# Performance work log

Hardware: AMD Instinct MI355X
Metric: run time of the kernel (lower is better)

The kernel has to match this reference:

```python
import jax, jax.numpy as jnp
import numpy as np


def setup_inputs() -> dict:
    key = jax.random.key(0)
    k1, k2 = jax.random.split(key)
    B, F, D = 4096, 32, 64
    P = F * (F - 1) // 2  # 496
    inputs = jax.random.normal(k1, (B, F, D), dtype=jnp.float32)
    W = jax.random.normal(k2, (P, D, D), dtype=jnp.float32) * 0.05
    return {"inputs": inputs, "W": W}


def reference(inputs, W):
    # inputs: (B, F, D); W: (P, D, D) with P = F*(F-1)/2 pairs in
    # itertools.combinations order (== np.triu_indices row-major order).
    F = inputs.shape[1]
    idx_i, idx_j = np.triu_indices(F, k=1)  # static pair indices
    vi = inputs[:, idx_i, :]                 # (B, P, D)
    vj = inputs[:, idx_j, :]                 # (B, P, D)
    # per-pair matmul v_i @ W_p, then elementwise multiply with v_j
    vidots = jnp.einsum('bpd,pde->bpe', vi, W)
    return vidots * vj                       # (B, P, D)
```

## Files before the change

kernel.cpp:

```cpp
#include <hip/hip_runtime.h>

#define Bsz 4096
#define Fsz 32
#define Dsz 64
#define Psz 496
#define RPW 64
#define WPB 4

__global__ __launch_bounds__(256, 4)
void bilinear_wreg_kernel(const float* __restrict__ in,
                          const float* __restrict__ W,
                          float* __restrict__ out)
{
    const int p    = blockIdx.x;
    const int tid  = threadIdx.x;
    const int lane = tid & 63;

    const int bb0 = __builtin_amdgcn_readfirstlane(
                        blockIdx.y * (RPW * WPB) + (tid >> 6) * RPW);

    int i = 0, rem = p;
    while (rem >= Fsz - 1 - i) { rem -= Fsz - 1 - i; ++i; }
    const int j = i + 1 + rem;

    float w[Dsz];
    {
        const float* Wp = W + (size_t)p * (Dsz * Dsz) + lane;
#pragma unroll
        for (int d = 0; d < Dsz; ++d) w[d] = Wp[(size_t)d * Dsz];
    }
#pragma unroll
    for (int d = 0; d < Dsz; ++d) {
        asm volatile("" : "+v"(w[d]));
    }

    const float* __restrict__ vi0 = in  + ((size_t)bb0 * Fsz + i) * Dsz;
    const float* __restrict__ vj0 = in  + ((size_t)bb0 * Fsz + j) * Dsz + lane;
    float*       __restrict__ op0 = out + ((size_t)bb0 * Psz + p) * Dsz + lane;

#pragma unroll 1
    for (int r = 0; r < RPW; ++r) {
        const float* vi  = vi0 + (size_t)r * (Fsz * Dsz);
        const float  vjv = vj0[(size_t)r * (Fsz * Dsz)];

        float s[Dsz];
#pragma unroll
        for (int d = 0; d < Dsz; ++d) s[d] = vi[d];

        float acc = 0.0f;
#pragma unroll
        for (int d = 0; d < Dsz; ++d) acc = fmaf(s[d], w[d], acc);

        __builtin_nontemporal_store(acc * vjv, op0 + (size_t)r * (Psz * Dsz));
    }
}

extern "C" void kernel_launch(void* const* d_in, const int* in_sizes, int n_in,
                              void* d_out, int out_size, void* d_ws, size_t ws_size,
                              hipStream_t stream) {
    const float* in  = (const float*)d_in[0];
    const float* W   = (const float*)d_in[1];
    float*       out = (float*)d_out;

    dim3 grid(Psz, Bsz / (RPW * WPB));
    bilinear_wreg_kernel<<<grid, 256, 0, stream>>>(in, W, out);
}
```

Before: 747.1 us.

## Stage W in shared memory and block over rows to cut register use

Stops holding the 64 W entries per lane in registers. Each block now copies the pair's W matrix into LDS with float4 loads and then reads it in chunks of eight. The loop processes eight batch rows at a time with separate accumulators, so each W chunk is reused across those rows. Launch bounds go from 4 to 8 blocks per CU to raise occupancy. In exchange the kernel adds LDS reads, a barrier, and 16KB of LDS per block, which may limit how many blocks fit on a CU.

New measurement: 1.320 ms. 76.6% more time.

```diff
diff --git a/kernel.cpp b/kernel.cpp
--- a/kernel.cpp
+++ b/kernel.cpp
@@ -6,12 +6,16 @@
 #define Psz 496
 #define RPW 64
 #define WPB 4
+#define RB  8
+#define DC  8
 
-__global__ __launch_bounds__(256, 4)
-void bilinear_wreg_kernel(const float* __restrict__ in,
+__global__ __launch_bounds__(256, 8)
+void bilinear_sblk_kernel(const float* __restrict__ in,
                           const float* __restrict__ W,
                           float* __restrict__ out)
 {
+    __shared__ float sW[Dsz][Dsz];
+
     const int p    = blockIdx.x;
     const int tid  = threadIdx.x;
     const int lane = tid & 63;
@@ -23,35 +27,45 @@
     while (rem >= Fsz - 1 - i) { rem -= Fsz - 1 - i; ++i; }
     const int j = i + 1 + rem;
 
-    float w[Dsz];
     {
-        const float* Wp = W + (size_t)p * (Dsz * Dsz) + lane;
+        const float4* gW  = (const float4*)(W + (size_t)p * Dsz * Dsz);
+        float4*       sWv = (float4*)(&sW[0][0]);
 #pragma unroll
-        for (int d = 0; d < Dsz; ++d) w[d] = Wp[(size_t)d * Dsz];
+        for (int k = 0; k < 4; ++k) sWv[tid + k * 256] = gW[tid + k * 256];
     }
-#pragma unroll
-    for (int d = 0; d < Dsz; ++d) {
-        asm volatile("" : "+v"(w[d]));
-    }
+    __syncthreads();
 
-    const float* __restrict__ vi0 = in  + ((size_t)bb0 * Fsz + i) * Dsz;
-    const float* __restrict__ vj0 = in  + ((size_t)bb0 * Fsz + j) * Dsz + lane;
-    float*       __restrict__ op0 = out + ((size_t)bb0 * Psz + p) * Dsz + lane;
+    const float* vib = in  + ((size_t)bb0 * Fsz + i) * Dsz;
+    const float* vjb = in  + ((size_t)bb0 * Fsz + j) * Dsz + lane;
+    float*       opb = out + ((size_t)bb0 * Psz + p) * Dsz + lane;
 
 #pragma unroll 1
-    for (int r = 0; r < RPW; ++r) {
-        const float* vi  = vi0 + (size_t)r * (Fsz * Dsz);
-        const float  vjv = vj0[(size_t)r * (Fsz * Dsz)];
+    for (int rb = 0; rb < RPW / RB; ++rb) {
+        float acc[RB];
+#pragma unroll
+        for (int r = 0; r < RB; ++r) acc[r] = 0.0f;
 
-        float s[Dsz];
 #pragma unroll
-        for (int d = 0; d < Dsz; ++d) s[d] = vi[d];
+        for (int dc = 0; dc < Dsz / DC; ++dc) {
+            float wv[DC];
+#pragma unroll
+            for (int k = 0; k < DC; ++k) wv[k] = sW[dc * DC + k][lane];
 
-        float acc = 0.0f;
 #pragma unroll
-        for (int d = 0; d < Dsz; ++d) acc = fmaf(s[d], w[d], acc);
+            for (int r = 0; r < RB; ++r) {
+                const size_t row_off = (size_t)(rb * RB + r) * (Fsz * Dsz);
+#pragma unroll
+                for (int k = 0; k < DC; ++k)
+                    acc[r] = fmaf(vib[row_off + dc * DC + k], wv[k], acc[r]);
+            }
+        }
 
-        __builtin_nontemporal_store(acc * vjv, op0 + (size_t)r * (Psz * Dsz));
+#pragma unroll
+        for (int r = 0; r < RB; ++r) {
+            const size_t ro = (size_t)(rb * RB + r);
+            __builtin_nontemporal_store(acc[r] * vjb[ro * (Fsz * Dsz)],
+                                        opb + ro * ((size_t)Psz * Dsz));
+        }
     }
 }
 
@@ -63,5 +77,5 @@
     float*       out = (float*)d_out;
 
     dim3 grid(Psz, Bsz / (RPW * WPB));
-    bilinear_wreg_kernel<<<grid, 256, 0, stream>>>(in, W, out);
+    bilinear_sblk_kernel<<<grid, 256, 0, stream>>>(in, W, out);
 }
```
